# Kernel optimization log

Measured on AMD Instinct MI355X. Metric: run time of the kernel, lower is better.

## Reference

```python
import jax, jax.numpy as jnp
import numpy as np

WORD_EMB_DIM = 100
TAG_EMB_DIM = 28
EMB_DIM = WORD_EMB_DIM + TAG_EMB_DIM  # 128; LSTM hidden size per direction
HID = EMB_DIM
WORD_VOCAB = 50000
TAG_VOCAB = 50
B = 16
L = 128


def _lstm_dir(x, w_ih, w_hh, b_ih, b_hh, reverse):
    # x: [B, T, In] -> [B, T, H]; PyTorch gate order i, f, g, o
    xT = jnp.swapaxes(x, 0, 1)  # [T, B, In]
    if reverse:
        xT = xT[::-1]
    xp = jnp.einsum('tbi,gi->tbg', xT, w_ih) + b_ih + b_hh  # [T, B, 4H]
    H = w_hh.shape[1]

    def step(carry, g_x):
        h, c = carry
        g = g_x + h @ w_hh.T
        i, f, gg, o = jnp.split(g, 4, axis=-1)
        c = jax.nn.sigmoid(f) * c + jax.nn.sigmoid(i) * jnp.tanh(gg)
        h = jax.nn.sigmoid(o) * jnp.tanh(c)
        return (h, c), h

    h0 = jnp.zeros((x.shape[0], H), x.dtype)
    _, hs = jax.lax.scan(step, (h0, h0), xp)
    if reverse:
        hs = hs[::-1]
    return jnp.swapaxes(hs, 0, 1)


def _bilstm(x, pf, pb):
    return jnp.concatenate([_lstm_dir(x, *pf, reverse=False),
                            _lstm_dir(x, *pb, reverse=True)], axis=-1)


def setup_inputs() -> dict:
    key = jax.random.key(0)
    ks = iter(jax.random.split(key, 40))

    def rn(shape, s=0.1):
        return (jax.random.normal(next(ks), shape) * s).astype(jnp.float32)

    inp = {
        'words_idx': jax.random.randint(next(ks), (B, L), 0, WORD_VOCAB),
        'pos_idx': jax.random.randint(next(ks), (B, L), 0, TAG_VOCAB),
        'max_length': L,
        'lengths': jax.random.randint(next(ks), (B,), 1, L + 1),
        'word_emb': rn((WORD_VOCAB, WORD_EMB_DIM)),
        'tag_emb': rn((TAG_VOCAB, TAG_EMB_DIM)),
    }
    for l, insz in ((0, EMB_DIM), (1, 2 * HID)):
        for d in ('f', 'b'):
            inp[f'w_ih_l{l}{d}'] = rn((4 * HID, insz))
            inp[f'w_hh_l{l}{d}'] = rn((4 * HID, HID))
            inp[f'b_ih_l{l}{d}'] = rn((4 * HID,))
            inp[f'b_hh_l{l}{d}'] = rn((4 * HID,))
    inp['fc1_w'] = rn((100, 4 * EMB_DIM))
    inp['fc1_b'] = rn((100,))
    inp['fc2_w'] = rn((1, 100))
    inp['fc2_b'] = rn((1,))
    return inp


def reference(words_idx, pos_idx, max_length, lengths, word_emb, tag_emb,
              w_ih_l0f, w_hh_l0f, b_ih_l0f, b_hh_l0f,
              w_ih_l0b, w_hh_l0b, b_ih_l0b, b_hh_l0b,
              w_ih_l1f, w_hh_l1f, b_ih_l1f, b_hh_l1f,
              w_ih_l1b, w_hh_l1b, b_ih_l1b, b_hh_l1b,
              fc1_w, fc1_b, fc2_w, fc2_b):
    # embeddings + concat -> [B, L, EMB_DIM]
    x = jnp.concatenate([word_emb[words_idx[:, :max_length]],
                         tag_emb[pos_idx[:, :max_length]]], axis=-1)
    h = _bilstm(x, (w_ih_l0f, w_hh_l0f, b_ih_l0f, b_hh_l0f),
                (w_ih_l0b, w_hh_l0b, b_ih_l0b, b_hh_l0b))
    h = _bilstm(h, (w_ih_l1f, w_hh_l1f, b_ih_l1f, b_hh_l1f),
                (w_ih_l1b, w_hh_l1b, b_ih_l1b, b_hh_l1b))  # [B, L, 2*HID]
    # Pairwise feature(i,j) = cat(h[:,i], h[:,j]); fuse fc1 by splitting its
    # weight into head/dependent halves -> broadcast-add instead of L^2 concat.
    D = h.shape[-1]
    wa, wb = fc1_w[:, :D], fc1_w[:, D:]
    a = jnp.einsum('bld,kd->blk', h, wa)                 # [B, L, 100]
    bp = jnp.einsum('bld,kd->blk', h, wb) + fc1_b        # [B, L, 100]
    hid = jnp.tanh(a[:, :, None, :] + bp[:, None, :, :])  # [B, L, L, 100]
    scores = jnp.einsum('bijk,ok->bijo', hid, fc2_w) + fc2_b  # [B, L, L, 1]
    # original stacks features along axis 0 in (i outer, j inner) order
    return scores.transpose(1, 2, 0, 3).reshape(max_length * max_length, -1, 1)
```

## Files before the change

kernel.cpp:

```cpp
#include <hip/hip_runtime.h>

typedef float v2f __attribute__((ext_vector_type(2)));
typedef _Float16 h2 __attribute__((ext_vector_type(2)));

__device__ __forceinline__ float frcp(float x){ return __builtin_amdgcn_rcpf(x); }
__device__ __forceinline__ float fexp2(float x){ return __builtin_amdgcn_exp2f(x); }
__device__ __forceinline__ float tanh_(float x){ return 1.f - 2.f*frcp(1.f + fexp2(2.8853900817779268f*x)); }

#if __has_builtin(__builtin_amdgcn_fdot2)
#define FDOT2(a,b,c) __builtin_amdgcn_fdot2((a),(b),(c),false)
#else
#define FDOT2(a,b,c) ((c) + (float)(a).x*(float)(b).x + (float)(a).y*(float)(b).y)
#endif

__global__ __launch_bounds__(256) void embed_kernel(
    const int* __restrict__ widx, const int* __restrict__ pidx,
    const float* __restrict__ wemb, const float* __restrict__ temb,
    float* __restrict__ x)
{
    int gid = blockIdx.x*256 + threadIdx.x;
    int bt = gid >> 7, c = gid & 127;
    float v;
    if (c < 100) v = wemb[(size_t)widx[bt]*100 + c];
    else         v = temb[(size_t)pidx[bt]*28 + (c-100)];
    x[gid] = v;
}

__global__ __launch_bounds__(256) void pack_kernel(
    const float* __restrict__ whh_f, const float* __restrict__ whh_b,
    unsigned* __restrict__ wpack)
{
    int id = blockIdx.x*256 + threadIdx.x;
    int d = id >> 15, t = (id >> 6) & 511, j = id & 63;
    const float* whh = d ? whh_b : whh_f;
    int r = t >> 2, g = t & 3;
    const float* src = whh + (size_t)(g*128 + r)*128 + 2*j;
    unsigned short a = __builtin_bit_cast(unsigned short, (_Float16)src[0]);
    unsigned short b = __builtin_bit_cast(unsigned short, (_Float16)src[1]);
    wpack[((size_t)d*512 + t)*64 + j] = (unsigned)a | ((unsigned)b << 16);
}

__global__ __launch_bounds__(256) void gemm_kernel(
    const float* __restrict__ A, int K,
    const float* __restrict__ B0, const float* __restrict__ B1, int ldb,
    const float* __restrict__ bias0a, const float* __restrict__ bias0b,
    const float* __restrict__ bias1a, const float* __restrict__ bias1b,
    float* __restrict__ C0, float* __restrict__ C1, int ldc, int N,
    int expflag, int permflag)
{
    __shared__ float As[16][140];
    __shared__ float Bs[16][68];
    const int z = blockIdx.z;
    const float* B  = z ? B1 : B0;
    const float* ba = z ? bias1a : bias0a;
    const float* bb = z ? bias1b : bias0b;
    float* C = z ? C1 : C0;
    const int m0 = blockIdx.x * 128;
    const int n0 = blockIdx.y * 64;
    const int tx = threadIdx.x;
    const int tm = tx & 15, tn = tx >> 4;
    const int arow = tx >> 1, akq = (tx & 1) * 8;
    const int brow = tx >> 2, bkq = (tx & 3) * 4;
    const int g_arow = arow + 4*(arow >> 5);
    const int rbase = tm*8 + 4*(tm >> 2);
    float acc[8][4];
    #pragma unroll
    for (int r=0;r<8;++r){
        #pragma unroll
        for (int c=0;c<4;++c) acc[r][c]=0.f; }
    const int bn = n0 + brow;
    const int brow_src = permflag ? ((bn & 3)*128 + (bn >> 2)) : bn;
    for (int k0 = 0; k0 < K; k0 += 16) {
        const float* ap = A + (size_t)(m0+arow)*K + k0 + akq;
        float4 a0 = *(const float4*)ap;
        float4 a1 = *(const float4*)(ap+4);
        float4 bv = make_float4(0.f,0.f,0.f,0.f);
        if (bn < N) {
            const float* bp = B + (size_t)brow_src*ldb + k0 + bkq;
            bv = *(const float4*)bp;
        }
        __syncthreads();
        As[akq+0][g_arow]=a0.x; As[akq+1][g_arow]=a0.y; As[akq+2][g_arow]=a0.z; As[akq+3][g_arow]=a0.w;
        As[akq+4][g_arow]=a1.x; As[akq+5][g_arow]=a1.y; As[akq+6][g_arow]=a1.z; As[akq+7][g_arow]=a1.w;
        Bs[bkq+0][brow]=bv.x; Bs[bkq+1][brow]=bv.y; Bs[bkq+2][brow]=bv.z; Bs[bkq+3][brow]=bv.w;
        __syncthreads();
        #pragma unroll
        for (int kk = 0; kk < 16; ++kk) {
            float4 av0 = *(const float4*)&As[kk][rbase];
            float4 av1 = *(const float4*)&As[kk][rbase+4];
            float4 bvv = *(const float4*)&Bs[kk][tn*4];
            float a[8] = {av0.x,av0.y,av0.z,av0.w,av1.x,av1.y,av1.z,av1.w};
            float b[4] = {bvv.x,bvv.y,bvv.z,bvv.w};
            #pragma unroll
            for (int r=0;r<8;++r){
                #pragma unroll
                for (int c=0;c<4;++c)
                    acc[r][c] = fmaf(a[r], b[c], acc[r][c]);
            }
        }
    }
    float bias[4];
    #pragma unroll
    for (int c=0;c<4;++c) {
        int n = n0 + tn*4 + c;
        int nsrc = permflag ? ((n & 3)*128 + (n >> 2)) : n;
        float v = 0.f;
        if (n < N) {
            if (ba) v += ba[nsrc];
            if (bb) v += bb[nsrc];
        }
        bias[c] = v;
    }
    #pragma unroll
    for (int r=0;r<8;++r) {
        int m = m0 + tm*8 + r;
        float v[4];
        #pragma unroll
        for (int c=0;c<4;++c) {
            float t = acc[r][c] + bias[c];
            if (expflag) t = fexp2(fminf(fmaxf(t,-40.f),40.f)*2.8853900817779268f);
            v[c] = t;
        }
        int n = n0 + tn*4;
        if (n + 3 < N) {
            float4 st; st.x=v[0]; st.y=v[1]; st.z=v[2]; st.w=v[3];
            *(float4*)&C[(size_t)m*ldc + n] = st;
        } else {
            #pragma unroll
            for (int c=0;c<4;++c) if (n+c < N) C[(size_t)m*ldc + n + c] = v[c];
        }
    }
}

__global__ __launch_bounds__(512, 2)
void lstm_kernel(
    const float* __restrict__ xp,
    const unsigned* wpk,
    float* hcat)
{
    const int b = blockIdx.x & 15;
    const int dir = blockIdx.x >> 4;
    const int t = threadIdx.x;
    const int gate = t & 3, r = t >> 2;
    const int lane = t & 63, qbase = lane & ~3;
    const float kexp = (gate == 2) ? 2.8853900817779268f : -1.4426950408889634f;
    const float mA   = (gate == 2) ? -2.f : 1.f;
    const float mB   = (gate == 2) ?  1.f : 0.f;

    h2 w[64];
    {
        const unsigned* wr = wpk + ((size_t)dir*512 + t)*64;
        #pragma unroll
        for (int j = 0; j < 64; j += 4) {
            uint4 u = *(const uint4*)(wr + j);
            w[j+0] = __builtin_bit_cast(h2, u.x);
            w[j+1] = __builtin_bit_cast(h2, u.y);
            w[j+2] = __builtin_bit_cast(h2, u.z);
            w[j+3] = __builtin_bit_cast(h2, u.w);
        }
    }

    __shared__ _Float16 h_lds[2][128];
    float c = 0.f;
    if (t < 128) h_lds[0][t] = (_Float16)0.f;
    __syncthreads();

    const float* xpd = xp + (size_t)dir*(2048*512) + (size_t)b*(128*512);
    float xpv = xpd[(dir ? 127 : 0)*512 + t];
    for (int s = 0; s < 128; ++s) {
        const int ts = dir ? (127 - s) : s;
        const int tsn = dir ? (126 - s < 0 ? 0 : 126 - s) : (s + 1 > 127 ? 127 : s + 1);
        float xnext = xpd[tsn*512 + t];
        const uint4* hb = (const uint4*)&h_lds[s & 1][0];
        float A0=0.f, A1=0.f, A2=0.f, A3=0.f;
        #pragma unroll
        for (int j = 0; j < 16; ++j) {
            uint4 u = hb[j];
            A0 = FDOT2(w[4*j+0], __builtin_bit_cast(h2, u.x), A0);
            A1 = FDOT2(w[4*j+1], __builtin_bit_cast(h2, u.y), A1);
            A2 = FDOT2(w[4*j+2], __builtin_bit_cast(h2, u.z), A2);
            A3 = FDOT2(w[4*j+3], __builtin_bit_cast(h2, u.w), A3);
        }
        float dot = xpv + ((A0+A1)+(A2+A3));
        float act = fmaf(mA, frcp(1.f + fexp2(kexp*dot)), mB);
        float i_ = __shfl(act, qbase+0, 64);
        float f_ = __shfl(act, qbase+1, 64);
        float g_ = __shfl(act, qbase+2, 64);
        float o_ = __shfl(act, qbase+3, 64);
        c = f_*c + i_*g_;
        float h = o_ * tanh_(c);
        if (gate == 0) {
            h_lds[(s & 1) ^ 1][r] = (_Float16)h;
            hcat[((size_t)b*128 + ts)*256 + dir*128 + r] = h;
        }
        xpv = xnext;
        __syncthreads();
    }
}

__global__ __launch_bounds__(256) void pair_kernel(
    const float* __restrict__ ea, const float* __restrict__ eb,
    const float* __restrict__ fc2w, const float* __restrict__ fc2b,
    float* __restrict__ out)
{
    __shared__ float eas[32][100];
    __shared__ float ebs[32][100];
    __shared__ float w2s[100];
    __shared__ float red[128];
    const int it = blockIdx.x * 32, jt = blockIdx.y * 32, b = blockIdx.z;
    const int tx = threadIdx.x;
    const float* eab = ea + (size_t)b*12800;
    const float* ebb = eb + (size_t)b*12800;
    for (int idx = tx; idx < 3200; idx += 256) {
        int r = idx / 100;
        int cc = idx - r*100;
        eas[r][cc] = eab[(it + r)*100 + cc];
        ebs[r][cc] = ebb[(jt + r)*100 + cc];
    }
    if (tx < 128) {
        float wv = (tx < 100) ? fc2w[tx] : 0.f;
        if (tx < 100) w2s[tx] = -2.f*wv;
        red[tx] = wv;
    }
    __syncthreads();
    for (int s2 = 64; s2 > 0; s2 >>= 1) {
        if (tx < s2) red[tx] += red[tx+s2];
        __syncthreads();
    }
    const float S = red[0] + fc2b[0];
    const int jp = tx & 15, ip = tx >> 4;
    const int i0 = ip*2, j0 = jp*2;
    float acc00=S, acc01=S, acc10=S, acc11=S;
    #pragma unroll
    for (int k = 0; k < 100; k += 4) {
        float4 A0 = *(const float4*)&eas[i0][k];
        float4 A1 = *(const float4*)&eas[i0+1][k];
        float4 B0 = *(const float4*)&ebs[j0][k];
        float4 B1 = *(const float4*)&ebs[j0+1][k];
        float4 W  = *(const float4*)&w2s[k];
        acc00 = fmaf(W.x, frcp(fmaf(A0.x,B0.x,1.f)), acc00);
        acc01 = fmaf(W.x, frcp(fmaf(A0.x,B1.x,1.f)), acc01);
        acc10 = fmaf(W.x, frcp(fmaf(A1.x,B0.x,1.f)), acc10);
        acc11 = fmaf(W.x, frcp(fmaf(A1.x,B1.x,1.f)), acc11);
        acc00 = fmaf(W.y, frcp(fmaf(A0.y,B0.y,1.f)), acc00);
        acc01 = fmaf(W.y, frcp(fmaf(A0.y,B1.y,1.f)), acc01);
        acc10 = fmaf(W.y, frcp(fmaf(A1.y,B0.y,1.f)), acc10);
        acc11 = fmaf(W.y, frcp(fmaf(A1.y,B1.y,1.f)), acc11);
        acc00 = fmaf(W.z, frcp(fmaf(A0.z,B0.z,1.f)), acc00);
        acc01 = fmaf(W.z, frcp(fmaf(A0.z,B1.z,1.f)), acc01);
        acc10 = fmaf(W.z, frcp(fmaf(A1.z,B0.z,1.f)), acc10);
        acc11 = fmaf(W.z, frcp(fmaf(A1.z,B1.z,1.f)), acc11);
        acc00 = fmaf(W.w, frcp(fmaf(A0.w,B0.w,1.f)), acc00);
        acc01 = fmaf(W.w, frcp(fmaf(A0.w,B1.w,1.f)), acc01);
        acc10 = fmaf(W.w, frcp(fmaf(A1.w,B0.w,1.f)), acc10);
        acc11 = fmaf(W.w, frcp(fmaf(A1.w,B1.w,1.f)), acc11);
    }
    const int gi0 = it + i0, gj0 = jt + j0;
    out[((size_t)(gi0  )*128 + gj0  )*16 + b] = acc00;
    out[((size_t)(gi0  )*128 + gj0+1)*16 + b] = acc01;
    out[((size_t)(gi0+1)*128 + gj0  )*16 + b] = acc10;
    out[((size_t)(gi0+1)*128 + gj0+1)*16 + b] = acc11;
}

extern "C" void kernel_launch(void* const* d_in, const int* in_sizes, int n_in,
                              void* d_out, int out_size, void* d_ws, size_t ws_size,
                              hipStream_t stream)
{
    (void)in_sizes; (void)n_in; (void)out_size; (void)ws_size;
    const int*   widx = (const int*)d_in[0];
    const int*   pidx = (const int*)d_in[1];
    const float* wemb = (const float*)d_in[4];
    const float* temb = (const float*)d_in[5];
    const float* w_ih_l0f = (const float*)d_in[6];
    const float* w_hh_l0f = (const float*)d_in[7];
    const float* b_ih_l0f = (const float*)d_in[8];
    const float* b_hh_l0f = (const float*)d_in[9];
    const float* w_ih_l0b = (const float*)d_in[10];
    const float* w_hh_l0b = (const float*)d_in[11];
    const float* b_ih_l0b = (const float*)d_in[12];
    const float* b_hh_l0b = (const float*)d_in[13];
    const float* w_ih_l1f = (const float*)d_in[14];
    const float* w_hh_l1f = (const float*)d_in[15];
    const float* b_ih_l1f = (const float*)d_in[16];
    const float* b_hh_l1f = (const float*)d_in[17];
    const float* w_ih_l1b = (const float*)d_in[18];
    const float* w_hh_l1b = (const float*)d_in[19];
    const float* b_ih_l1b = (const float*)d_in[20];
    const float* b_hh_l1b = (const float*)d_in[21];
    const float* fc1_w = (const float*)d_in[22];
    const float* fc1_b = (const float*)d_in[23];
    const float* fc2_w = (const float*)d_in[24];
    const float* fc2_b = (const float*)d_in[25];

    float* ws  = (float*)d_ws;
    float* x   = ws;
    float* xp0 = x + 262144;
    float* h1  = xp0 + 2097152;
    float* xp1 = h1 + 524288;
    float* h2  = xp1 + 2097152;
    float* ea  = h2 + 524288;
    float* eb  = ea + 204800;
    unsigned* wpk0 = (unsigned*)(eb + 204800);
    unsigned* wpk1 = wpk0 + 65536;

    embed_kernel<<<1024, 256, 0, stream>>>(widx, pidx, wemb, temb, x);
    pack_kernel<<<256, 256, 0, stream>>>(w_hh_l0f, w_hh_l0b, wpk0);
    pack_kernel<<<256, 256, 0, stream>>>(w_hh_l1f, w_hh_l1b, wpk1);
    gemm_kernel<<<dim3(16,8,2), 256, 0, stream>>>(x, 128,
        w_ih_l0f, w_ih_l0b, 128,
        b_ih_l0f, b_hh_l0f, b_ih_l0b, b_hh_l0b,
        xp0, xp0 + 1048576, 512, 512, 0, 1);
    lstm_kernel<<<32, 512, 0, stream>>>(xp0, wpk0, h1);
    gemm_kernel<<<dim3(16,8,2), 256, 0, stream>>>(h1, 256,
        w_ih_l1f, w_ih_l1b, 256,
        b_ih_l1f, b_hh_l1f, b_ih_l1b, b_hh_l1b,
        xp1, xp1 + 1048576, 512, 512, 0, 1);
    lstm_kernel<<<32, 512, 0, stream>>>(xp1, wpk1, h2);
    gemm_kernel<<<dim3(16,2,2), 256, 0, stream>>>(h2, 256,
        fc1_w, fc1_w + 256, 512,
        nullptr, nullptr, fc1_b, nullptr,
        ea, eb, 100, 100, 1, 0);
    pair_kernel<<<dim3(4,4,16), 256, 0, stream>>>(ea, eb, fc2_w, fc2_b, (float*)d_out);
}
```

Before: 359.3 us.

## Split LSTM recurrent dot product across two threads per gate row

Each gate row's 128-element recurrent dot product is now split across two threads (1024 threads per block instead of 512). A shfl_xor combines the two halves, and the gate-gather shuffles are remapped to match. This halves the serial FDOT2 chain per step and the weight registers per thread, which should shorten the per-timestep critical path of the latency-bound recurrence. The cost is an extra cross-lane shuffle per step, a larger block to synchronize each step, and doubled redundant xp loads.

```diff
diff --git a/kernel.cpp b/kernel.cpp
--- a/kernel.cpp
+++ b/kernel.cpp
@@ -132,64 +132,62 @@
     }
 }
 
-__global__ __launch_bounds__(512, 2)
+__global__ __launch_bounds__(1024, 1)
 void lstm_kernel(
     const float* __restrict__ xp,
-    const unsigned* wpk,
+    const unsigned* __restrict__ wpk,
     float* hcat)
 {
     const int b = blockIdx.x & 15;
     const int dir = blockIdx.x >> 4;
-    const int t = threadIdx.x;
-    const int gate = t & 3, r = t >> 2;
-    const int lane = t & 63, qbase = lane & ~3;
+    const int tt = threadIdx.x;
+    const int gr = tt >> 1;
+    const int kh = tt & 1;
+    const int gate = gr & 3, r = gr >> 2;
+    const int lbase = (tt & 63) & ~7;
     const float kexp = (gate == 2) ? 2.8853900817779268f : -1.4426950408889634f;
     const float mA   = (gate == 2) ? -2.f : 1.f;
     const float mB   = (gate == 2) ?  1.f : 0.f;
 
-    h2 w[64];
+    uint4 W0,W1,W2,W3,W4,W5,W6,W7;
     {
-        const unsigned* wr = wpk + ((size_t)dir*512 + t)*64;
-        #pragma unroll
-        for (int j = 0; j < 64; j += 4) {
-            uint4 u = *(const uint4*)(wr + j);
-            w[j+0] = __builtin_bit_cast(h2, u.x);
-            w[j+1] = __builtin_bit_cast(h2, u.y);
-            w[j+2] = __builtin_bit_cast(h2, u.z);
-            w[j+3] = __builtin_bit_cast(h2, u.w);
-        }
+        const uint4* wr = (const uint4*)(wpk + (((size_t)dir*512 + gr)*64 + (kh << 5)));
+        W0 = wr[0]; W1 = wr[1]; W2 = wr[2]; W3 = wr[3];
+        W4 = wr[4]; W5 = wr[5]; W6 = wr[6]; W7 = wr[7];
     }
 
     __shared__ _Float16 h_lds[2][128];
     float c = 0.f;
-    if (t < 128) h_lds[0][t] = (_Float16)0.f;
+    if (tt < 128) h_lds[0][tt] = (_Float16)0.f;
     __syncthreads();
 
     const float* xpd = xp + (size_t)dir*(2048*512) + (size_t)b*(128*512);
-    float xpv = xpd[(dir ? 127 : 0)*512 + t];
+    float xpv = xpd[(dir ? 127 : 0)*512 + gr];
     for (int s = 0; s < 128; ++s) {
         const int ts = dir ? (127 - s) : s;
         const int tsn = dir ? (126 - s < 0 ? 0 : 126 - s) : (s + 1 > 127 ? 127 : s + 1);
-        float xnext = xpd[tsn*512 + t];
-        const uint4* hb = (const uint4*)&h_lds[s & 1][0];
+        float xnext = xpd[tsn*512 + gr];
+        const uint4* hb = (const uint4*)((const char*)&h_lds[s & 1][0] + (kh << 7));
         float A0=0.f, A1=0.f, A2=0.f, A3=0.f;
-        #pragma unroll
-        for (int j = 0; j < 16; ++j) {
-            uint4 u = hb[j];
-            A0 = FDOT2(w[4*j+0], __builtin_bit_cast(h2, u.x), A0);
-            A1 = FDOT2(w[4*j+1], __builtin_bit_cast(h2, u.y), A1);
-            A2 = FDOT2(w[4*j+2], __builtin_bit_cast(h2, u.z), A2);
-            A3 = FDOT2(w[4*j+3], __builtin_bit_cast(h2, u.w), A3);
-        }
-        float dot = xpv + ((A0+A1)+(A2+A3));
+        #define DOT4(WV, J) { uint4 u = hb[J]; \
+            A0 = FDOT2(__builtin_bit_cast(h2, WV.x), __builtin_bit_cast(h2, u.x), A0); \
+            A1 = FDOT2(__builtin_bit_cast(h2, WV.y), __builtin_bit_cast(h2, u.y), A1); \
+            A2 = FDOT2(__builtin_bit_cast(h2, WV.z), __builtin_bit_cast(h2, u.z), A2); \
+            A3 = FDOT2(__builtin_bit_cast(h2, WV.w), __builtin_bit_cast(h2, u.w), A3); }
+        DOT4(W0,0) DOT4(W1,1) DOT4(W2,2) DOT4(W3,3)
+        DOT4(W4,4) DOT4(W5,5) DOT4(W6,6) DOT4(W7,7)
+        #undef DOT4
+        float half = (A0+A1)+(A2+A3);
+        half += __shfl_xor(half, 1, 64);
+        float dot = xpv + half;
         float act = fmaf(mA, frcp(1.f + fexp2(kexp*dot)), mB);
-        float i_ = __shfl(act, qbase+0, 64);
-        float f_ = __shfl(act, qbase+1, 64);
-        float g_ = __shfl(act, qbase+2, 64);
-        float o_ = __shfl(act, qbase+3, 64);
+        float i_ = __shfl(act, lbase+0, 64);
+        float f_ = __shfl(act, lbase+2, 64);
+        float g_ = __shfl(act, lbase+4, 64);
+        float o_ = __shfl(act, lbase+6, 64);
         c = f_*c + i_*g_;
         float h = o_ * tanh_(c);
-        if (gate == 0) {
+        if ((tt & 7) == 0) {
             h_lds[(s & 1) ^ 1][r] = (_Float16)h;
             hcat[((size_t)b*128 + ts)*256 + dir*128 + r] = h;
         }
@@ -310,12 +308,12 @@
         w_ih_l0f, w_ih_l0b, 128,
         b_ih_l0f, b_hh_l0f, b_ih_l0b, b_hh_l0b,
         xp0, xp0 + 1048576, 512, 512, 0, 1);
-    lstm_kernel<<<32, 512, 0, stream>>>(xp0, wpk0, h1);
+    lstm_kernel<<<32, 1024, 0, stream>>>(xp0, wpk0, h1);
     gemm_kernel<<<dim3(16,8,2), 256, 0, stream>>>(h1, 256,
         w_ih_l1f, w_ih_l1b, 256,
         b_ih_l1f, b_hh_l1f, b_ih_l1b, b_hh_l1b,
         xp1, xp1 + 1048576, 512, 512, 0, 1);
-    lstm_kernel<<<32, 512, 0, stream>>>(xp1, wpk1, h2);
+    lstm_kernel<<<32, 1024, 0, stream>>>(xp1, wpk1, h2);
     gemm_kernel<<<dim3(16,2,2), 256, 0, stream>>>(h2, 256,
         fc1_w, fc1_w + 256, 512,
         nullptr, nullptr, fc1_b, nullptr,
```

Measured after the change: 405.2 us. 12.8% more time.
